# Performance work log

Measured on AMD Instinct MI355X. Metric: run time of the kernel, lower is better.

## Reference

```python
import jax, jax.numpy as jnp
import numpy as np

B, S, D_MODEL, D_FF, NUM_EXPERTS, TOP_K = 2, 2048, 1024, 4096, 8, 2


def setup_inputs() -> dict:
    key = jax.random.key(0)
    ks = jax.random.split(key, 5)
    scale = 0.02
    return {
        "x": jax.random.normal(ks[0], (B, S, D_MODEL), jnp.float32),
        # gate: Linear(d_model, num_experts, bias=False); stored as [d_model, E]
        "Wg": jax.random.normal(ks[1], (D_MODEL, NUM_EXPERTS), jnp.float32) * scale,
        # stacked expert FFN params
        "W1": jax.random.normal(ks[2], (NUM_EXPERTS, D_MODEL, D_FF), jnp.float32) * scale,
        "b1": jnp.zeros((NUM_EXPERTS, D_FF), jnp.float32),
        "W2": jax.random.normal(ks[3], (NUM_EXPERTS, D_FF, D_MODEL), jnp.float32) * scale,
        "b2": jnp.zeros((NUM_EXPERTS, D_MODEL), jnp.float32),
    }


def _moe_forward(x, Wg, W1, b1, W2, b2):
    b, s, d = x.shape
    xt = x.reshape(-1, d)                       # [T, d]
    T = xt.shape[0]
    # --- TopKRouter ---
    probs = jax.nn.softmax(xt @ Wg, axis=-1)    # [T, E]
    w, idx = jax.lax.top_k(probs, TOP_K)        # [T, K]
    w = w / jnp.sum(w, axis=-1, keepdims=True)  # renormalize top-k weights
    # scatter routing weights into dense per-expert combine weights [T, E]
    gate = jnp.zeros((T, Wg.shape[1]), xt.dtype)
    gate = gate.at[jnp.arange(T)[:, None], idx].add(w)
    # --- per-expert FFN, weighted combine (scan over experts, E is small) ---
    def body(out, params):
        W1e, b1e, W2e, b2e, ge = params
        h = jax.nn.relu(xt @ W1e + b1e)         # [T, d_ff]
        out = out + (h @ W2e + b2e) * ge[:, None]
        return out, None
    out0 = jnp.zeros_like(xt)
    out, _ = jax.lax.scan(body, out0, (W1, b1, W2, b2, gate.T))
    return out.reshape(b, s, d)


def reference(x, Wg, W1, b1, W2, b2):
    # eval mode: dropout = identity, load-balance loss = None -> return output only
    return _moe_forward(x, Wg, W1, b1, W2, b2)
```

## Files before the change

kernel.cpp:

```cpp
#include <hip/hip_runtime.h>
#include <hip/hip_bf16.h>
#include <cstdint>
#include <cstddef>

#define T_TOK 4096
#define DM 1024
#define DFF 4096
#define NE 8
#define BT 128
#define BK 64
#define PADCAP (T_TOK * 2 + NE * BT)
#define MTILES (PADCAP / BT)

typedef __attribute__((ext_vector_type(8))) short short8;
typedef __attribute__((ext_vector_type(4))) float f32x4;

__device__ __forceinline__ unsigned short f2bf(float f) {
  unsigned int u = __float_as_uint(f);
  return (unsigned short)((u + 0x7fff + ((u >> 16) & 1)) >> 16);
}

__device__ __forceinline__ void load_lds16(const void* g, void* l) {
  __builtin_amdgcn_global_load_lds(
      (const __attribute__((address_space(1))) int*)g,
      (__attribute__((address_space(3))) int*)l, 16, 0, 0);
}

__global__ __launch_bounds__(256) void gate_kernel(
    const float* __restrict__ x, const float* __restrict__ Wg,
    int* __restrict__ counts, int* __restrict__ topk_idx,
    float* __restrict__ topk_w, unsigned short* __restrict__ xb) {
  int gid = blockIdx.x * blockDim.x + threadIdx.x;
  int t = gid >> 6;
  int lane = gid & 63;
  if (t >= T_TOK) return;
  const float* xr = x + (size_t)t * DM;
  unsigned short* xbr = xb + (size_t)t * DM;
  float acc[NE];
#pragma unroll
  for (int e = 0; e < NE; ++e) acc[e] = 0.f;
#pragma unroll
  for (int j = 0; j < DM / 64; ++j) {
    int d = lane + j * 64;
    float xv = xr[d];
    xbr[d] = f2bf(xv);
    const float4* wr = (const float4*)(Wg + (size_t)d * NE);
    float4 w0 = wr[0], w1 = wr[1];
    acc[0] += xv * w0.x; acc[1] += xv * w0.y;
    acc[2] += xv * w0.z; acc[3] += xv * w0.w;
    acc[4] += xv * w1.x; acc[5] += xv * w1.y;
    acc[6] += xv * w1.z; acc[7] += xv * w1.w;
  }
#pragma unroll
  for (int off = 32; off >= 1; off >>= 1) {
#pragma unroll
    for (int e = 0; e < NE; ++e) acc[e] += __shfl_xor(acc[e], off, 64);
  }
  if (lane == 0) {
    int i0 = 0;
#pragma unroll
    for (int e = 1; e < NE; ++e)
      if (acc[e] > acc[i0]) i0 = e;
    int i1 = (i0 == 0) ? 1 : 0;
#pragma unroll
    for (int e = 0; e < NE; ++e)
      if (e != i0 && acc[e] > acc[i1]) i1 = e;
    float e1 = __expf(acc[i1] - acc[i0]);
    float inv = 1.f / (1.f + e1);
    topk_idx[t * 2] = i0;
    topk_idx[t * 2 + 1] = i1;
    topk_w[t * 2] = inv;
    topk_w[t * 2 + 1] = e1 * inv;
    atomicAdd(&counts[i0], 1);
    atomicAdd(&counts[i1], 1);
  }
}

__global__ void init_kernel(int* counts, int* cursors, int* bucket_tok) {
  int i = blockIdx.x * blockDim.x + threadIdx.x;
  if (i < NE) { counts[i] = 0; cursors[i] = 0; }
  if (i < PADCAP) bucket_tok[i] = -1;
}

__global__ void offsets_kernel(const int* __restrict__ counts,
                               int* __restrict__ offsets) {
  if (threadIdx.x == 0) {
    int o = 0;
    offsets[0] = 0;
    for (int e = 0; e < NE; ++e) {
      o += (counts[e] + BT - 1) & ~(BT - 1);
      offsets[e + 1] = o;
    }
  }
}

__global__ void scatter_kernel(const int* __restrict__ topk_idx,
                               const float* __restrict__ topk_w,
                               const int* __restrict__ offsets,
                               int* __restrict__ cursors,
                               int* __restrict__ bucket_tok,
                               float* __restrict__ bucket_w) {
  int t = blockIdx.x * blockDim.x + threadIdx.x;
  if (t >= T_TOK) return;
#pragma unroll
  for (int k = 0; k < 2; ++k) {
    int e = topk_idx[t * 2 + k];
    float w = topk_w[t * 2 + k];
    int pos = atomicAdd(&cursors[e], 1);
    int slot = offsets[e] + pos;
    bucket_tok[slot] = t;
    bucket_w[slot] = w;
  }
}

__global__ __launch_bounds__(256) void transpose_cvt_kernel(
    const float* __restrict__ W, unsigned short* __restrict__ Wt,
    int K, int N) {
  __shared__ float Ls[64][68];
  int e = blockIdx.z;
  const float* We = W + (size_t)e * K * N;
  unsigned short* Wte = Wt + (size_t)e * K * N;
  int k0 = blockIdx.x * 64, n0 = blockIdx.y * 64;
  int tid = threadIdx.x;
  int kr = tid >> 4, nf = (tid & 15) * 4;
#pragma unroll
  for (int p = 0; p < 4; ++p) {
    int k = kr + p * 16;
    float4 v = *(const float4*)(We + (size_t)(k0 + k) * N + n0 + nf);
    Ls[k][nf] = v.x; Ls[k][nf + 1] = v.y;
    Ls[k][nf + 2] = v.z; Ls[k][nf + 3] = v.w;
  }
  __syncthreads();
#pragma unroll
  for (int i = 0; i < 2; ++i) {
    int id = tid + i * 256;
    int n = id >> 3, kc = id & 7;
    short8 hv;
#pragma unroll
    for (int j = 0; j < 8; ++j) hv[j] = (short)f2bf(Ls[kc * 8 + j][n]);
    *(short8*)(Wte + (size_t)(n0 + n) * K + k0 + kc * 8) = hv;
  }
}


__global__ __launch_bounds__(256) void gemm1_kernel(
    const unsigned short* __restrict__ xb, const unsigned short* __restrict__ Wt1,
    const float* __restrict__ b1, const int* __restrict__ offsets,
    const int* __restrict__ bucket_tok, unsigned short* __restrict__ h) {
  int r0 = blockIdx.x * BT;
  if (r0 >= offsets[NE]) return;
  int e = 0;
  while (offsets[e + 1] <= r0) ++e;
  int n0 = blockIdx.y * 128;

  __shared__ __align__(16) short As[128 * 64];
  __shared__ __align__(16) short Bs[128 * 64];
  __shared__ int toks[BT];

  int tid = threadIdx.x;
  if (tid < BT) toks[tid] = bucket_tok[r0 + tid];
  __syncthreads();

  int lane = tid & 63, w = tid >> 6;
  int rsub = lane >> 3, kc = lane & 7;
  int jsw = (kc ^ rsub) * 8;
  const unsigned short* aptr[4];
  const unsigned short* bptr[4];
#pragma unroll
  for (int i = 0; i < 4; ++i) {
    int m = w * 32 + i * 8 + rsub;
    int tk = toks[m]; if (tk < 0) tk = 0;
    aptr[i] = xb + (size_t)tk * DM + jsw;
    bptr[i] = Wt1 + ((size_t)e * DFF + n0 + m) * DM + jsw;
  }
  int ldsA = w * 2048 + lane * 8;

  int wm = w & 1, wn = w >> 1;
  int g = lane >> 4, l15 = lane & 15;
  int x7 = l15 & 7;
  int csel0 = ((g) ^ x7) * 8;
  int csel1 = ((4 + g) ^ x7) * 8;

  f32x4 acc[4][4];
#pragma unroll
  for (int i = 0; i < 4; ++i)
#pragma unroll
    for (int jj = 0; jj < 4; ++jj) acc[i][jj] = (f32x4){0.f, 0.f, 0.f, 0.f};

  for (int k0 = 0; k0 < DM; k0 += BK) {
#pragma unroll
    for (int i = 0; i < 4; ++i) {
      load_lds16(aptr[i] + k0, &As[ldsA + i * 512]);
      load_lds16(bptr[i] + k0, &Bs[ldsA + i * 512]);
    }
    __syncthreads();
#pragma unroll
    for (int ks = 0; ks < 2; ++ks) {
      int cs = ks ? csel1 : csel0;
      short8 af[4], bfr[4];
#pragma unroll
      for (int mi = 0; mi < 4; ++mi)
        af[mi] = *(const short8*)&As[(wm * 64 + mi * 16 + l15) * 64 + cs];
#pragma unroll
      for (int nj = 0; nj < 4; ++nj)
        bfr[nj] = *(const short8*)&Bs[(wn * 64 + nj * 16 + l15) * 64 + cs];
#pragma unroll
      for (int mi = 0; mi < 4; ++mi)
#pragma unroll
        for (int nj = 0; nj < 4; ++nj)
          acc[mi][nj] = __builtin_amdgcn_mfma_f32_16x16x32_bf16(
              af[mi], bfr[nj], acc[mi][nj], 0, 0, 0);
    }
    __syncthreads();
  }

  const float* b1e = b1 + (size_t)e * DFF;
#pragma unroll
  for (int nj = 0; nj < 4; ++nj) {
    int n = n0 + wn * 64 + nj * 16 + l15;
    float bv = b1e[n];
#pragma unroll
    for (int mi = 0; mi < 4; ++mi) {
      int mb = r0 + wm * 64 + mi * 16 + g * 4;
#pragma unroll
      for (int r = 0; r < 4; ++r) {
        float v = acc[mi][nj][r] + bv;
        h[(size_t)(mb + r) * DFF + n] = f2bf(fmaxf(v, 0.f));
      }
    }
  }
}

__global__ __launch_bounds__(256) void gemm2_kernel(
    const unsigned short* __restrict__ h, const unsigned short* __restrict__ Wt2,
    const float* __restrict__ b2, const int* __restrict__ offsets,
    const int* __restrict__ bucket_tok, const float* __restrict__ bucket_w,
    float* __restrict__ out) {
  int r0 = blockIdx.x * BT;
  if (r0 >= offsets[NE]) return;
  int e = 0;
  while (offsets[e + 1] <= r0) ++e;
  int n0 = blockIdx.y * 128;
  int kbeg = blockIdx.z * (DFF / 2);

  __shared__ __align__(16) short As[128 * 64];
  __shared__ __align__(16) short Bs[128 * 64];
  __shared__ int toks[BT];
  __shared__ float wts[BT];

  int tid = threadIdx.x;
  if (tid < BT) {
    toks[tid] = bucket_tok[r0 + tid];
    wts[tid] = bucket_w[r0 + tid];
  }
  __syncthreads();

  int lane = tid & 63, w = tid >> 6;
  int rsub = lane >> 3, kc = lane & 7;
  int jsw = (kc ^ rsub) * 8;
  const unsigned short* aptr[4];
  const unsigned short* bptr[4];
#pragma unroll
  for (int i = 0; i < 4; ++i) {
    int m = w * 32 + i * 8 + rsub;
    aptr[i] = h + ((size_t)(r0 + m)) * DFF + jsw;
    bptr[i] = Wt2 + ((size_t)e * DM + n0 + m) * DFF + jsw;
  }
  int ldsA = w * 2048 + lane * 8;

  int wm = w & 1, wn = w >> 1;
  int g = lane >> 4, l15 = lane & 15;
  int x7 = l15 & 7;
  int csel0 = ((g) ^ x7) * 8;
  int csel1 = ((4 + g) ^ x7) * 8;

  f32x4 acc[4][4];
#pragma unroll
  for (int i = 0; i < 4; ++i)
#pragma unroll
    for (int jj = 0; jj < 4; ++jj) acc[i][jj] = (f32x4){0.f, 0.f, 0.f, 0.f};

  for (int k0 = kbeg; k0 < kbeg + DFF / 2; k0 += BK) {
#pragma unroll
    for (int i = 0; i < 4; ++i) {
      load_lds16(aptr[i] + k0, &As[ldsA + i * 512]);
      load_lds16(bptr[i] + k0, &Bs[ldsA + i * 512]);
    }
    __syncthreads();
#pragma unroll
    for (int ks = 0; ks < 2; ++ks) {
      int cs = ks ? csel1 : csel0;
      short8 af[4], bfr[4];
#pragma unroll
      for (int mi = 0; mi < 4; ++mi)
        af[mi] = *(const short8*)&As[(wm * 64 + mi * 16 + l15) * 64 + cs];
#pragma unroll
      for (int nj = 0; nj < 4; ++nj)
        bfr[nj] = *(const short8*)&Bs[(wn * 64 + nj * 16 + l15) * 64 + cs];
#pragma unroll
      for (int mi = 0; mi < 4; ++mi)
#pragma unroll
        for (int nj = 0; nj < 4; ++nj)
          acc[mi][nj] = __builtin_amdgcn_mfma_f32_16x16x32_bf16(
              af[mi], bfr[nj], acc[mi][nj], 0, 0, 0);
    }
    __syncthreads();
  }

  const float* b2e = b2 + (size_t)e * DM;
  float bscale = (blockIdx.z == 0) ? 1.f : 0.f;
#pragma unroll
  for (int nj = 0; nj < 4; ++nj) {
    int n = n0 + wn * 64 + nj * 16 + l15;
    float bv = b2e[n] * bscale;
#pragma unroll
    for (int mi = 0; mi < 4; ++mi) {
      int mb = wm * 64 + mi * 16 + g * 4;
#pragma unroll
      for (int r = 0; r < 4; ++r) {
        int m = mb + r;
        int tk = toks[m];
        if (tk < 0) continue;
        atomicAdd(&out[(size_t)tk * DM + n],
                  (acc[mi][nj][r] + bv) * wts[m]);
      }
    }
  }
}

extern "C" void kernel_launch(void* const* d_in, const int* in_sizes, int n_in,
                              void* d_out, int out_size, void* d_ws,
                              size_t ws_size, hipStream_t stream) {
  const float* x = (const float*)d_in[0];
  const float* Wg = (const float*)d_in[1];
  const float* W1 = (const float*)d_in[2];
  const float* b1 = (const float*)d_in[3];
  const float* W2 = (const float*)d_in[4];
  const float* b2 = (const float*)d_in[5];
  float* out = (float*)d_out;

  int* ws_i = (int*)d_ws;
  int* counts = ws_i;
  int* offsets = ws_i + 8;
  int* cursors = ws_i + 20;
  int* bucket_tok = ws_i + 32;
  float* bucket_w = (float*)(ws_i + 32 + PADCAP);
  int* topk_idx = ws_i + 32 + 2 * PADCAP;
  float* topk_w = (float*)(ws_i + 32 + 2 * PADCAP + 2 * T_TOK);

  const size_t XB_OFF = 1u << 20;
  const size_t WT_OFF = XB_OFF + (size_t)T_TOK * DM * 2;
  const size_t H_OFF = WT_OFF + (size_t)NE * DM * DFF * 2;
  unsigned short* xb = (unsigned short*)((char*)d_ws + XB_OFF);
  unsigned short* Wt = (unsigned short*)((char*)d_ws + WT_OFF);
  unsigned short* h = (unsigned short*)((char*)d_ws + H_OFF);

  hipMemsetAsync(d_out, 0, (size_t)T_TOK * DM * sizeof(float), stream);
  init_kernel<<<(PADCAP + 255) / 256, 256, 0, stream>>>(counts, cursors,
                                                        bucket_tok);
  gate_kernel<<<T_TOK / 4, 256, 0, stream>>>(x, Wg, counts, topk_idx, topk_w,
                                             xb);
  offsets_kernel<<<1, 64, 0, stream>>>(counts, offsets);
  scatter_kernel<<<T_TOK / 256, 256, 0, stream>>>(topk_idx, topk_w, offsets,
                                                  cursors, bucket_tok, bucket_w);
  transpose_cvt_kernel<<<dim3(DM / 64, DFF / 64, NE), 256, 0, stream>>>(
      W1, Wt, DM, DFF);
  gemm1_kernel<<<dim3(MTILES, DFF / 128), 256, 0, stream>>>(
      xb, Wt, b1, offsets, bucket_tok, h);
  transpose_cvt_kernel<<<dim3(DFF / 64, DM / 64, NE), 256, 0, stream>>>(
      W2, Wt, DFF, DM);
  gemm2_kernel<<<dim3(MTILES, DM / 128, 2), 256, 0, stream>>>(
      h, Wt, b2, offsets, bucket_tok, bucket_w, out);
}
```

Measured before the change: 742.8 us.

## Double-buffer GEMM LDS loads and replace atomic scatter with bf16 staging plus combine

Both expert GEMMs now double-buffer their shared-memory tiles, issuing the next K-slice's global-to-LDS loads before computing the current one, and wait with explicit vmcnt waits and barriers. gemm2 no longer does atomicAdd into the output. It writes its per-split-K partial results as bf16 to a staging buffer indexed by slot, and a new combine kernel gathers each token's two expert slots, sums the split halves, applies the routing weights and writes the output once. The grid is reordered so the N/split index varies fastest. This removes the output memset and the fp32 atomics, at the cost of extra staging traffic, an extra launch and bf16 rounding of the partial sums.

```diff
diff --git a/kernel.cpp b/kernel.cpp
--- a/kernel.cpp
+++ b/kernel.cpp
@@ -19,12 +19,24 @@
   unsigned int u = __float_as_uint(f);
   return (unsigned short)((u + 0x7fff + ((u >> 16) & 1)) >> 16);
 }
+__device__ __forceinline__ float bf2f(unsigned short u) {
+  return __uint_as_float((unsigned int)u << 16);
+}
 
 __device__ __forceinline__ void load_lds16(const void* g, void* l) {
   __builtin_amdgcn_global_load_lds(
       (const __attribute__((address_space(1))) int*)g,
       (__attribute__((address_space(3))) int*)l, 16, 0, 0);
 }
+
+#define WAIT_VM8() __builtin_amdgcn_s_waitcnt(0x0F78)
+#define WAIT_VM0() __builtin_amdgcn_s_waitcnt(0x0F70)
+#define BARRIER()                          \
+  do {                                     \
+    __asm__ volatile("" ::: "memory");     \
+    __builtin_amdgcn_s_barrier();          \
+    __asm__ volatile("" ::: "memory");     \
+  } while (0)
 
 __global__ __launch_bounds__(256) void gate_kernel(
     const float* __restrict__ x, const float* __restrict__ Wg,
@@ -95,21 +107,19 @@
 }
 
 __global__ void scatter_kernel(const int* __restrict__ topk_idx,
-                               const float* __restrict__ topk_w,
                                const int* __restrict__ offsets,
                                int* __restrict__ cursors,
                                int* __restrict__ bucket_tok,
-                               float* __restrict__ bucket_w) {
+                               int* __restrict__ slot_of) {
   int t = blockIdx.x * blockDim.x + threadIdx.x;
   if (t >= T_TOK) return;
 #pragma unroll
   for (int k = 0; k < 2; ++k) {
     int e = topk_idx[t * 2 + k];
-    float w = topk_w[t * 2 + k];
     int pos = atomicAdd(&cursors[e], 1);
     int slot = offsets[e] + pos;
     bucket_tok[slot] = t;
-    bucket_w[slot] = w;
+    slot_of[t * 2 + k] = slot;
   }
 }
 
@@ -153,8 +163,8 @@
   while (offsets[e + 1] <= r0) ++e;
   int n0 = blockIdx.y * 128;
 
-  __shared__ __align__(16) short As[128 * 64];
-  __shared__ __align__(16) short Bs[128 * 64];
+  __shared__ __align__(16) short As[2 * 128 * 64];
+  __shared__ __align__(16) short Bs[2 * 128 * 64];
   __shared__ int toks[BT];
 
   int tid = threadIdx.x;
@@ -164,21 +174,21 @@
   int lane = tid & 63, w = tid >> 6;
   int rsub = lane >> 3, kc = lane & 7;
   int jsw = (kc ^ rsub) * 8;
-  const unsigned short* aptr[4];
-  const unsigned short* bptr[4];
+  const unsigned short* ga[4];
+  const unsigned short* gb[4];
 #pragma unroll
   for (int i = 0; i < 4; ++i) {
     int m = w * 32 + i * 8 + rsub;
     int tk = toks[m]; if (tk < 0) tk = 0;
-    aptr[i] = xb + (size_t)tk * DM + jsw;
-    bptr[i] = Wt1 + ((size_t)e * DFF + n0 + m) * DM + jsw;
-  }
-  int ldsA = w * 2048 + lane * 8;
+    ga[i] = xb + (size_t)tk * DM + jsw;
+    gb[i] = Wt1 + ((size_t)e * DFF + n0 + m) * DM + jsw;
+  }
+  int ldsW = w * 2048 + lane * 8;
 
   int wm = w & 1, wn = w >> 1;
   int g = lane >> 4, l15 = lane & 15;
   int x7 = l15 & 7;
-  int csel0 = ((g) ^ x7) * 8;
+  int csel0 = (g ^ x7) * 8;
   int csel1 = ((4 + g) ^ x7) * 8;
 
   f32x4 acc[4][4];
@@ -187,23 +197,39 @@
 #pragma unroll
     for (int jj = 0; jj < 4; ++jj) acc[i][jj] = (f32x4){0.f, 0.f, 0.f, 0.f};
 
-  for (int k0 = 0; k0 < DM; k0 += BK) {
-#pragma unroll
-    for (int i = 0; i < 4; ++i) {
-      load_lds16(aptr[i] + k0, &As[ldsA + i * 512]);
-      load_lds16(bptr[i] + k0, &Bs[ldsA + i * 512]);
-    }
-    __syncthreads();
+#pragma unroll
+  for (int i = 0; i < 4; ++i) {
+    load_lds16(ga[i], &As[ldsW + i * 512]);
+    load_lds16(gb[i], &Bs[ldsW + i * 512]);
+  }
+
+  int buf = 0;
+  const int NIT = DM / BK;
+  for (int it = 0; it < NIT; ++it) {
+    if (it + 1 < NIT) {
+      int ko = (it + 1) * BK;
+      int dst = (buf ^ 1) * 8192 + ldsW;
+#pragma unroll
+      for (int i = 0; i < 4; ++i) {
+        load_lds16(ga[i] + ko, &As[dst + i * 512]);
+        load_lds16(gb[i] + ko, &Bs[dst + i * 512]);
+      }
+      WAIT_VM8();
+    } else {
+      WAIT_VM0();
+    }
+    BARRIER();
+    int bb = buf * 8192;
 #pragma unroll
     for (int ks = 0; ks < 2; ++ks) {
       int cs = ks ? csel1 : csel0;
       short8 af[4], bfr[4];
 #pragma unroll
       for (int mi = 0; mi < 4; ++mi)
-        af[mi] = *(const short8*)&As[(wm * 64 + mi * 16 + l15) * 64 + cs];
+        af[mi] = *(const short8*)&As[bb + (wm * 64 + mi * 16 + l15) * 64 + cs];
 #pragma unroll
       for (int nj = 0; nj < 4; ++nj)
-        bfr[nj] = *(const short8*)&Bs[(wn * 64 + nj * 16 + l15) * 64 + cs];
+        bfr[nj] = *(const short8*)&Bs[bb + (wn * 64 + nj * 16 + l15) * 64 + cs];
 #pragma unroll
       for (int mi = 0; mi < 4; ++mi)
 #pragma unroll
@@ -211,7 +237,8 @@
           acc[mi][nj] = __builtin_amdgcn_mfma_f32_16x16x32_bf16(
               af[mi], bfr[nj], acc[mi][nj], 0, 0, 0);
     }
-    __syncthreads();
+    BARRIER();
+    buf ^= 1;
   }
 
   const float* b1e = b1 + (size_t)e * DFF;
@@ -234,44 +261,36 @@
 __global__ __launch_bounds__(256) void gemm2_kernel(
     const unsigned short* __restrict__ h, const unsigned short* __restrict__ Wt2,
     const float* __restrict__ b2, const int* __restrict__ offsets,
-    const int* __restrict__ bucket_tok, const float* __restrict__ bucket_w,
-    float* __restrict__ out) {
-  int r0 = blockIdx.x * BT;
+    unsigned short* __restrict__ S) {
+  int r0 = blockIdx.y * BT;
   if (r0 >= offsets[NE]) return;
   int e = 0;
   while (offsets[e + 1] <= r0) ++e;
-  int n0 = blockIdx.y * 128;
-  int kbeg = blockIdx.z * (DFF / 2);
-
-  __shared__ __align__(16) short As[128 * 64];
-  __shared__ __align__(16) short Bs[128 * 64];
-  __shared__ int toks[BT];
-  __shared__ float wts[BT];
+  int n0 = (blockIdx.x & 7) * 128;
+  int z = blockIdx.x >> 3;
+  int kbeg = z * (DFF / 2);
+
+  __shared__ __align__(16) short As[2 * 128 * 64];
+  __shared__ __align__(16) short Bs[2 * 128 * 64];
 
   int tid = threadIdx.x;
-  if (tid < BT) {
-    toks[tid] = bucket_tok[r0 + tid];
-    wts[tid] = bucket_w[r0 + tid];
-  }
-  __syncthreads();
-
   int lane = tid & 63, w = tid >> 6;
   int rsub = lane >> 3, kc = lane & 7;
   int jsw = (kc ^ rsub) * 8;
-  const unsigned short* aptr[4];
-  const unsigned short* bptr[4];
+  const unsigned short* ga[4];
+  const unsigned short* gb[4];
 #pragma unroll
   for (int i = 0; i < 4; ++i) {
     int m = w * 32 + i * 8 + rsub;
-    aptr[i] = h + ((size_t)(r0 + m)) * DFF + jsw;
-    bptr[i] = Wt2 + ((size_t)e * DM + n0 + m) * DFF + jsw;
-  }
-  int ldsA = w * 2048 + lane * 8;
+    ga[i] = h + ((size_t)(r0 + m)) * DFF + kbeg + jsw;
+    gb[i] = Wt2 + ((size_t)e * DM + n0 + m) * DFF + kbeg + jsw;
+  }
+  int ldsW = w * 2048 + lane * 8;
 
   int wm = w & 1, wn = w >> 1;
   int g = lane >> 4, l15 = lane & 15;
   int x7 = l15 & 7;
-  int csel0 = ((g) ^ x7) * 8;
+  int csel0 = (g ^ x7) * 8;
   int csel1 = ((4 + g) ^ x7) * 8;
 
   f32x4 acc[4][4];
@@ -280,23 +299,39 @@
 #pragma unroll
     for (int jj = 0; jj < 4; ++jj) acc[i][jj] = (f32x4){0.f, 0.f, 0.f, 0.f};
 
-  for (int k0 = kbeg; k0 < kbeg + DFF / 2; k0 += BK) {
-#pragma unroll
-    for (int i = 0; i < 4; ++i) {
-      load_lds16(aptr[i] + k0, &As[ldsA + i * 512]);
-      load_lds16(bptr[i] + k0, &Bs[ldsA + i * 512]);
-    }
-    __syncthreads();
+#pragma unroll
+  for (int i = 0; i < 4; ++i) {
+    load_lds16(ga[i], &As[ldsW + i * 512]);
+    load_lds16(gb[i], &Bs[ldsW + i * 512]);
+  }
+
+  int buf = 0;
+  const int NIT = (DFF / 2) / BK;
+  for (int it = 0; it < NIT; ++it) {
+    if (it + 1 < NIT) {
+      int ko = (it + 1) * BK;
+      int dst = (buf ^ 1) * 8192 + ldsW;
+#pragma unroll
+      for (int i = 0; i < 4; ++i) {
+        load_lds16(ga[i] + ko, &As[dst + i * 512]);
+        load_lds16(gb[i] + ko, &Bs[dst + i * 512]);
+      }
+      WAIT_VM8();
+    } else {
+      WAIT_VM0();
+    }
+    BARRIER();
+    int bb = buf * 8192;
 #pragma unroll
     for (int ks = 0; ks < 2; ++ks) {
       int cs = ks ? csel1 : csel0;
       short8 af[4], bfr[4];
 #pragma unroll
       for (int mi = 0; mi < 4; ++mi)
-        af[mi] = *(const short8*)&As[(wm * 64 + mi * 16 + l15) * 64 + cs];
+        af[mi] = *(const short8*)&As[bb + (wm * 64 + mi * 16 + l15) * 64 + cs];
 #pragma unroll
       for (int nj = 0; nj < 4; ++nj)
-        bfr[nj] = *(const short8*)&Bs[(wn * 64 + nj * 16 + l15) * 64 + cs];
+        bfr[nj] = *(const short8*)&Bs[bb + (wn * 64 + nj * 16 + l15) * 64 + cs];
 #pragma unroll
       for (int mi = 0; mi < 4; ++mi)
 #pragma unroll
@@ -304,28 +339,49 @@
           acc[mi][nj] = __builtin_amdgcn_mfma_f32_16x16x32_bf16(
               af[mi], bfr[nj], acc[mi][nj], 0, 0, 0);
     }
-    __syncthreads();
+    BARRIER();
+    buf ^= 1;
   }
 
   const float* b2e = b2 + (size_t)e * DM;
-  float bscale = (blockIdx.z == 0) ? 1.f : 0.f;
+  float bscale = (z == 0) ? 1.f : 0.f;
+  unsigned short* Sz = S + (size_t)z * PADCAP * DM;
 #pragma unroll
   for (int nj = 0; nj < 4; ++nj) {
     int n = n0 + wn * 64 + nj * 16 + l15;
     float bv = b2e[n] * bscale;
 #pragma unroll
     for (int mi = 0; mi < 4; ++mi) {
-      int mb = wm * 64 + mi * 16 + g * 4;
-#pragma unroll
-      for (int r = 0; r < 4; ++r) {
-        int m = mb + r;
-        int tk = toks[m];
-        if (tk < 0) continue;
-        atomicAdd(&out[(size_t)tk * DM + n],
-                  (acc[mi][nj][r] + bv) * wts[m]);
-      }
-    }
-  }
+      int mb = r0 + wm * 64 + mi * 16 + g * 4;
+#pragma unroll
+      for (int r = 0; r < 4; ++r)
+        Sz[(size_t)(mb + r) * DM + n] = f2bf(acc[mi][nj][r] + bv);
+    }
+  }
+}
+
+__global__ __launch_bounds__(256) void combine_kernel(
+    const unsigned short* __restrict__ S, const int* __restrict__ slot_of,
+    const float* __restrict__ topk_w, float* __restrict__ out) {
+  int gid = blockIdx.x * 256 + threadIdx.x;
+  int t = gid >> 7;
+  int c = (gid & 127) * 8;
+  int s0 = slot_of[t * 2], s1 = slot_of[t * 2 + 1];
+  float w0 = topk_w[t * 2], w1 = topk_w[t * 2 + 1];
+  const short8 a0 = *(const short8*)(S + (size_t)s0 * DM + c);
+  const short8 a1 = *(const short8*)(S + ((size_t)PADCAP + s0) * DM + c);
+  const short8 b0 = *(const short8*)(S + (size_t)s1 * DM + c);
+  const short8 b1 = *(const short8*)(S + ((size_t)PADCAP + s1) * DM + c);
+  float o[8];
+#pragma unroll
+  for (int j = 0; j < 8; ++j) {
+    float va = bf2f((unsigned short)a0[j]) + bf2f((unsigned short)a1[j]);
+    float vb = bf2f((unsigned short)b0[j]) + bf2f((unsigned short)b1[j]);
+    o[j] = w0 * va + w1 * vb;
+  }
+  float* op = out + (size_t)t * DM + c;
+  *(float4*)op = (float4){o[0], o[1], o[2], o[3]};
+  *(float4*)(op + 4) = (float4){o[4], o[5], o[6], o[7]};
 }
 
 extern "C" void kernel_launch(void* const* d_in, const int* in_sizes, int n_in,
@@ -344,31 +400,33 @@
   int* offsets = ws_i + 8;
   int* cursors = ws_i + 20;
   int* bucket_tok = ws_i + 32;
-  float* bucket_w = (float*)(ws_i + 32 + PADCAP);
-  int* topk_idx = ws_i + 32 + 2 * PADCAP;
-  float* topk_w = (float*)(ws_i + 32 + 2 * PADCAP + 2 * T_TOK);
+  int* topk_idx = ws_i + 32 + PADCAP;
+  float* topk_w = (float*)(ws_i + 32 + PADCAP + 2 * T_TOK);
+  int* slot_of = ws_i + 32 + PADCAP + 4 * T_TOK;
 
   const size_t XB_OFF = 1u << 20;
   const size_t WT_OFF = XB_OFF + (size_t)T_TOK * DM * 2;
   const size_t H_OFF = WT_OFF + (size_t)NE * DM * DFF * 2;
+  const size_t S_OFF = H_OFF + (size_t)PADCAP * DFF * 2;
   unsigned short* xb = (unsigned short*)((char*)d_ws + XB_OFF);
   unsigned short* Wt = (unsigned short*)((char*)d_ws + WT_OFF);
   unsigned short* h = (unsigned short*)((char*)d_ws + H_OFF);
-
-  hipMemsetAsync(d_out, 0, (size_t)T_TOK * DM * sizeof(float), stream);
+  unsigned short* S = (unsigned short*)((char*)d_ws + S_OFF);
+
   init_kernel<<<(PADCAP + 255) / 256, 256, 0, stream>>>(counts, cursors,
                                                         bucket_tok);
   gate_kernel<<<T_TOK / 4, 256, 0, stream>>>(x, Wg, counts, topk_idx, topk_w,
                                              xb);
   offsets_kernel<<<1, 64, 0, stream>>>(counts, offsets);
-  scatter_kernel<<<T_TOK / 256, 256, 0, stream>>>(topk_idx, topk_w, offsets,
-                                                  cursors, bucket_tok, bucket_w);
+  scatter_kernel<<<T_TOK / 256, 256, 0, stream>>>(topk_idx, offsets, cursors,
+                                                  bucket_tok, slot_of);
   transpose_cvt_kernel<<<dim3(DM / 64, DFF / 64, NE), 256, 0, stream>>>(
       W1, Wt, DM, DFF);
   gemm1_kernel<<<dim3(MTILES, DFF / 128), 256, 0, stream>>>(
       xb, Wt, b1, offsets, bucket_tok, h);
   transpose_cvt_kernel<<<dim3(DFF / 64, DM / 64, NE), 256, 0, stream>>>(
       W2, Wt, DFF, DM);
-  gemm2_kernel<<<dim3(MTILES, DM / 128, 2), 256, 0, stream>>>(
-      h, Wt, b2, offsets, bucket_tok, bucket_w, out);
-}
+  gemm2_kernel<<<dim3(16, MTILES), 256, 0, stream>>>(h, Wt, b2, offsets, S);
+  combine_kernel<<<(T_TOK * DM / 8) / 256, 256, 0, stream>>>(S, slot_of,
+                                                             topk_w, out);
+}
```

New measurement: 710.9 us. 4.3% less time.
